# Performance work log

Measured on AMD Instinct MI355X. Metric: run time of the kernel, lower is better.

Reference implementation:

```python
import jax, jax.numpy as jnp
import numpy as np

N = 4096            # num nodes
D = 256             # feature dim
NUM_SUPER_NODES = 6
THRESHOLD = 0.0
EPS = 1e-10
DENSITY = 0.02      # pre-symmetrization edge density


def setup_inputs() -> dict:
    key = jax.random.key(0)
    kx, ka = jax.random.split(key)
    X = jax.random.normal(kx, (N, D), dtype=jnp.float32)
    U = jax.random.uniform(ka, (N, N), dtype=jnp.float32)
    A = (U < DENSITY).astype(jnp.float32)
    A = jnp.maximum(A, A.T)                      # symmetric 0/1 adjacency
    A = A * (1.0 - jnp.eye(N, dtype=jnp.float32))  # no self-loops
    return {"X": X, "A": A}


def _greedy_labels(sim_np, n, num_super, threshold):
    """Sequential greedy union-find merge over pairs sorted by similarity.
    Matches torch: stable descending sort on sim only; merge until
    n - merged <= num_super; relabel roots in first-occurrence order.
    Inherently sequential/data-dependent -> done in numpy on concrete values
    (the torch original also detaches via .item())."""
    iu, ju = np.triu_indices(n, k=1)
    sims = sim_np[iu, ju]
    keep = sims >= threshold
    iu, ju, sims = iu[keep], ju[keep], sims[keep]
    order = np.argsort(-sims, kind="stable")     # stable desc == list.sort(reverse=True)
    parent = np.arange(n)

    def find(i):
        while parent[i] != i:
            parent[i] = parent[parent[i]]        # path halving
            i = parent[i]
        return i

    merged = 0
    for k in order:
        pi, pj = find(int(iu[k])), find(int(ju[k]))
        if pi != pj:
            parent[pj] = pi
            merged += 1
            if n - merged <= num_super:
                break
    mapping = {}
    labels = np.empty(n, dtype=np.int64)
    nl = 0
    for i in range(n):
        r = find(i)
        if r not in mapping:
            mapping[r] = nl
            nl += 1
        labels[i] = mapping[r]
    return labels, nl


def _build_P(A):
    """Vectorized pairwise Jaccard (replaces O(n^2) python loop) + greedy merge."""
    n = A.shape[0]
    A_bin = (A > 0).astype(jnp.float32)
    deg = A_bin.sum(axis=1)                      # |N(i)|
    inter = A_bin @ A_bin.T                      # [n,n] pairwise |Ni & Nj|
    union = deg[:, None] + deg[None, :] - inter  # |Ni | Nj|
    sim = jnp.where(union > 0, inter / jnp.maximum(union, 1.0), 0.0)
    labels, m = _greedy_labels(np.asarray(sim), n, NUM_SUPER_NODES, THRESHOLD)
    P_prime = jax.nn.one_hot(jnp.asarray(labels), m, dtype=jnp.float32)  # [n, m]
    sizes = P_prime.sum(axis=0)
    return P_prime / jnp.sqrt(sizes + EPS)[None, :]   # P = P' @ diag(1/sqrt(sizes+eps))


def reference(X, A):
    P = _build_P(A)                               # [n, m], m == NUM_SUPER_NODES
    X_coarse = P.T @ X                            # [m, D]
    A_coarse = P.T @ A @ P                        # [m, m]
    return (X_coarse, A_coarse, P)
```

## Files before the change

### kernel.cpp

```cpp
#include <hip/hip_runtime.h>

typedef unsigned long long u64;
typedef unsigned short u16;
typedef unsigned char u8;

#define NN 4096
#define NCH 64
#define NSUP 6

__device__ __forceinline__ u64 gkey(int v, int u, unsigned sb) {
  int i = v < u ? v : u, j = v < u ? u : v;
  unsigned idx = (unsigned)i * (unsigned)(2 * NN - i - 1) / 2u + (unsigned)(j - i - 1);
  return ((u64)sb << 24) | (u64)(0xFFFFFFu - idx);
}

__device__ __forceinline__ void ins4(u64& a0, u64& a1, u64& a2, u64& a3, u64 kk) {
  bool g0 = kk > a0, g1 = kk > a1, g2 = kk > a2, g3 = kk > a3;
  a3 = g3 ? (g2 ? a2 : kk) : a3;
  a2 = g2 ? (g1 ? a1 : kk) : a2;
  a1 = g1 ? (g0 ? a0 : kk) : a1;
  a0 = g0 ? kk : a0;
}

__global__ __launch_bounds__(256) void k_packdeg(const float* __restrict__ A,
                                                 u64* __restrict__ bits,
                                                 u16* __restrict__ deg,
                                                 float* out, int out_n,
                                                 int* comp, int* ncomp, int* mstcnt) {
  int t = threadIdx.x;
  int w = t >> 6, lane = t & 63;
  int row = blockIdx.x * 4 + w;
  const float* rp = A + (size_t)row * NN;
  u64 my = 0;
  int dsum = 0;
#pragma unroll 8
  for (int k = 0; k < 64; ++k) {
    float v = rp[k * 64 + lane];
    u64 m = __ballot(v > 0.0f);
    dsum += __popcll(m);
    if (lane == k) my = m;
  }
  bits[(size_t)row * NCH + lane] = my;
  if (lane == 0) deg[row] = (u16)dsum;
  int g = blockIdx.x * 256 + t;
  if (g < out_n) out[g] = 0.0f;
  if (g < NN) comp[g] = g;
  if (g == 0) { *ncomp = NN; *mstcnt = 0; }
}

__global__ __launch_bounds__(256) void k_inter(const u64* __restrict__ bits,
                                               u8* __restrict__ inter) {
  __shared__ ulonglong2 L[2][64 * 16];
  int b = blockIdx.x;
  int by = (int)((129.0f - sqrtf(16641.0f - 8.0f * (float)b)) * 0.5f) - 1;
  if (by < 0) by = 0;
#define CUM(y) (64 * (y) - ((y) * ((y) - 1)) / 2)
  while (by < 63 && CUM(by + 1) <= b) ++by;
  while (CUM(by) > b) --by;
  int bx = by + (b - CUM(by));
#undef CUM
  int i0 = by * 64, j0 = bx * 64;
  int t = threadIdx.x;
  int tx = t & 15, ty = t >> 4;
  int rowA[4], swA[4], rowB[4], swB[4];
#pragma unroll
  for (int a = 0; a < 4; ++a) {
    rowA[a] = ty * 4 + a; swA[a] = (rowA[a] ^ (rowA[a] >> 2)) & 7;
    rowB[a] = tx * 4 + a; swB[a] = (rowB[a] ^ (rowB[a] >> 2)) & 7;
  }
  int cuL = t & 15, rg = t >> 4;
  int acc[4][4] = {};
  for (int st = 0; st < 2; ++st) {
    __syncthreads();
#pragma unroll
    for (int rr = 0; rr < 4; ++rr) {
      int row = rg * 4 + rr;
      int sw = (row ^ (row >> 2)) & 7;
      L[0][row * 16 + (cuL ^ sw)] =
          reinterpret_cast<const ulonglong2*>(bits + (size_t)(i0 + row) * NCH)[st * 16 + cuL];
      L[1][row * 16 + (cuL ^ sw)] =
          reinterpret_cast<const ulonglong2*>(bits + (size_t)(j0 + row) * NCH)[st * 16 + cuL];
    }
    __syncthreads();
    for (int cu = 0; cu < 16; ++cu) {
      ulonglong2 av[4], bv[4];
#pragma unroll
      for (int a = 0; a < 4; ++a) av[a] = L[0][rowA[a] * 16 + (cu ^ swA[a])];
#pragma unroll
      for (int b2 = 0; b2 < 4; ++b2) bv[b2] = L[1][rowB[b2] * 16 + (cu ^ swB[b2])];
#pragma unroll
      for (int a = 0; a < 4; ++a)
#pragma unroll
        for (int b2 = 0; b2 < 4; ++b2)
          acc[a][b2] += __popcll(av[a].x & bv[b2].x) + __popcll(av[a].y & bv[b2].y);
    }
  }
#pragma unroll
  for (int a = 0; a < 4; ++a) {
    int i = i0 + ty * 4 + a;
    uchar4 wv;
    wv.x = (u8)acc[a][0]; wv.y = (u8)acc[a][1];
    wv.z = (u8)acc[a][2]; wv.w = (u8)acc[a][3];
    *reinterpret_cast<uchar4*>(inter + (size_t)i * NN + j0 + tx * 4) = wv;
  }
  if (bx != by) {
#pragma unroll
    for (int b2 = 0; b2 < 4; ++b2) {
      int j = j0 + tx * 4 + b2;
      uchar4 wv;
      wv.x = (u8)acc[0][b2]; wv.y = (u8)acc[1][b2];
      wv.z = (u8)acc[2][b2]; wv.w = (u8)acc[3][b2];
      *reinterpret_cast<uchar4*>(inter + (size_t)j * NN + i0 + ty * 4) = wv;
    }
  }
}

__global__ __launch_bounds__(256) void k_scan0(const u8* __restrict__ inter,
                                               const u16* __restrict__ deg,
                                               u64* __restrict__ tk,
                                               u64* __restrict__ nkey,
                                               int* __restrict__ nu) {
  __shared__ u16 deg_s[NN];
  int t = threadIdx.x;
  for (int i = t; i < NN / 8; i += 256)
    reinterpret_cast<uint4*>(deg_s)[i] = reinterpret_cast<const uint4*>(deg)[i];
  __syncthreads();
  int w = t >> 6, lane = t & 63;
  int v = blockIdx.x * 4 + w;
  int dv = (int)deg_s[v];
  const u8* row = inter + (size_t)v * NN;
  u64 a0 = 0, a1 = 0, a2 = 0, a3 = 0;
  for (int it = 0; it < 4; ++it) {
    int ub = it * 1024 + lane * 16;
    uint4 pv = *reinterpret_cast<const uint4*>(row + ub);
    uint4 dg0 = reinterpret_cast<const uint4*>(deg_s)[ub >> 3];
    uint4 dg1 = reinterpret_cast<const uint4*>(deg_s)[(ub >> 3) + 1];
    unsigned pw[4] = { pv.x, pv.y, pv.z, pv.w };
    unsigned dw[8] = { dg0.x, dg0.y, dg0.z, dg0.w, dg1.x, dg1.y, dg1.z, dg1.w };
#pragma unroll
    for (int k = 0; k < 16; ++k) {
      int u = ub + k;
      int iv = (int)((pw[k >> 2] >> ((k & 3) * 8)) & 0xFF);
      int du = (int)((dw[k >> 1] >> ((k & 1) * 16)) & 0xFFFF);
      int un = dv + du - iv;
      float s = (un > 0) ? ((float)iv / (float)un) : 0.0f;
      u64 kk = (u != v)
                   ? (((u64)__float_as_uint(s) << 32) | (u64)(0xFFFFFFFFu - (unsigned)u))
                   : 0ull;
      ins4(a0, a1, a2, a3, kk);
    }
  }
#pragma unroll
  for (int off = 1; off < 64; off <<= 1) {
    u64 b0 = __shfl_xor(a0, off, 64);
    u64 b1 = __shfl_xor(a1, off, 64);
    u64 b2 = __shfl_xor(a2, off, 64);
    u64 b3 = __shfl_xor(a3, off, 64);
    ins4(a0, a1, a2, a3, b0);
    ins4(a0, a1, a2, a3, b1);
    ins4(a0, a1, a2, a3, b2);
    ins4(a0, a1, a2, a3, b3);
  }
  if (lane == 0) {
    u64* tv = tk + (size_t)v * 4;
    tv[0] = a0; tv[1] = a1; tv[2] = a2; tv[3] = a3;
    int u0 = (int)(0xFFFFFFFFu - (unsigned)(a0 & 0xFFFFFFFFull));
    nkey[v] = gkey(v, u0, (unsigned)(a0 >> 32));
    nu[v] = u0;
  }
}

__global__ __launch_bounds__(256) void k_scan(const u8* __restrict__ inter,
                                              const u16* __restrict__ deg,
                                              const u64* __restrict__ tk,
                                              const int* __restrict__ comp,
                                              const int* __restrict__ ncomp,
                                              u64* __restrict__ nkey,
                                              int* __restrict__ nu) {
  if (*ncomp <= 1) return;
  __shared__ u16 comp_s[NN];
  __shared__ u16 deg_s[NN];
  __shared__ int anyneed;
  int t = threadIdx.x;
  if (t == 0) anyneed = 0;
  for (int i = t; i < NN / 8; i += 256) {
    int4 ca = reinterpret_cast<const int4*>(comp)[i * 2];
    int4 cb = reinterpret_cast<const int4*>(comp)[i * 2 + 1];
    uint4 pk;
    pk.x = (unsigned)ca.x | ((unsigned)ca.y << 16);
    pk.y = (unsigned)ca.z | ((unsigned)ca.w << 16);
    pk.z = (unsigned)cb.x | ((unsigned)cb.y << 16);
    pk.w = (unsigned)cb.z | ((unsigned)cb.w << 16);
    reinterpret_cast<uint4*>(comp_s)[i] = pk;
  }
  __syncthreads();
  int w = t >> 6, lane = t & 63;
  int v = blockIdx.x * 4 + w;
  int cv = (int)comp_s[v];
  u64 gk = 0; int bu = -1; bool need = true;
  const u64* tv = tk + (size_t)v * 4;
#pragma unroll
  for (int e = 0; e < 4; ++e) {
    u64 cand = tv[e];
    unsigned uu = 0xFFFFFFFFu - (unsigned)(cand & 0xFFFFFFFFull);
    if (need && (int)comp_s[uu] != cv) {
      need = false;
      gk = gkey(v, (int)uu, (unsigned)(cand >> 32));
      bu = (int)uu;
    }
  }
  if (!need) {
    if (lane == 0) { nkey[v] = gk; nu[v] = bu; }
  } else if (lane == 0) {
    atomicOr(&anyneed, 1 << w);
  }
  __syncthreads();
  int needmask = anyneed;
  if (!needmask) return;
  for (int i = t; i < NN / 8; i += 256)
    reinterpret_cast<uint4*>(deg_s)[i] = reinterpret_cast<const uint4*>(deg)[i];
  __syncthreads();
  if (!(needmask >> w & 1)) return;
  int dv = (int)deg_s[v];
  const u8* row = inter + (size_t)v * NN;
  u64 key = 0;
  for (int it = 0; it < 4; ++it) {
    int ub = it * 1024 + lane * 16;
    uint4 pv = *reinterpret_cast<const uint4*>(row + ub);
    uint4 dg0 = reinterpret_cast<const uint4*>(deg_s)[ub >> 3];
    uint4 dg1 = reinterpret_cast<const uint4*>(deg_s)[(ub >> 3) + 1];
    uint4 cs0 = reinterpret_cast<const uint4*>(comp_s)[ub >> 3];
    uint4 cs1 = reinterpret_cast<const uint4*>(comp_s)[(ub >> 3) + 1];
    unsigned pw[4] = { pv.x, pv.y, pv.z, pv.w };
    unsigned dw[8] = { dg0.x, dg0.y, dg0.z, dg0.w, dg1.x, dg1.y, dg1.z, dg1.w };
    unsigned cw[8] = { cs0.x, cs0.y, cs0.z, cs0.w, cs1.x, cs1.y, cs1.z, cs1.w };
#pragma unroll
    for (int k = 0; k < 16; ++k) {
      int iv = (int)((pw[k >> 2] >> ((k & 3) * 8)) & 0xFF);
      int du = (int)((dw[k >> 1] >> ((k & 1) * 16)) & 0xFFFF);
      int cu = (int)((cw[k >> 1] >> ((k & 1) * 16)) & 0xFFFF);
      int un = dv + du - iv;
      float s = (un > 0) ? ((float)iv / (float)un) : 0.0f;
      u64 kk = (cu != cv)
                   ? (((u64)__float_as_uint(s) << 32) | (u64)(0xFFFFFFFFu - (unsigned)(ub + k)))
                   : 0ull;
      if (kk > key) key = kk;
    }
  }
#pragma unroll
  for (int off = 32; off > 0; off >>= 1) {
    unsigned lo = (unsigned)key, hi = (unsigned)(key >> 32);
    unsigned olo = __shfl_xor(lo, off, 64), ohi = __shfl_xor(hi, off, 64);
    u64 o = ((u64)ohi << 32) | (u64)olo;
    if (o > key) key = o;
  }
  if (lane == 0) {
    u64 pk = 0; int u = -1;
    if (key != 0ull) {
      unsigned simb = (unsigned)(key >> 32);
      u = (int)(0xFFFFFFFFu - (unsigned)(key & 0xFFFFFFFFull));
      pk = gkey(v, u, simb);
    }
    nkey[v] = pk; nu[v] = u;
  }
}

__global__ __launch_bounds__(1024) void k_merge(const u64* __restrict__ nkey,
                                                const int* __restrict__ nu,
                                                int* comp, int* ncomp, int* mstcnt,
                                                u64* mkey, int* mi, int* mj,
                                                int* labels_g, float* invs_g, float* out) {
  if (*ncomp <= 1) return;
  __shared__ int parent_s[NN];
  __shared__ u64 cbest_s[NN];
  __shared__ unsigned char mk_s[NN];
  __shared__ int roots[16];
  __shared__ int rcnt, cnt_s, chg_s, changed;
  __shared__ int szs[8];
  __shared__ float ivs[8];
  int t = threadIdx.x;
  for (int c = t; c < NN; c += 1024) { parent_s[c] = c; cbest_s[c] = 0ull; }
  __syncthreads();
  for (int v = t; v < NN; v += 1024) {
    u64 k = nkey[v];
    if (k) atomicMax(&cbest_s[comp[v]], k);
  }
  __syncthreads();
  for (int v = t; v < NN; v += 1024) {
    u64 k = nkey[v];
    if (!k) continue;
    int c = comp[v];
    if (k == cbest_s[c]) {
      int u = nu[v];
      int cu = comp[u];
      bool mutual = (cbest_s[cu] == k);
      if (!mutual || v < u) {
        int slot = atomicAdd(mstcnt, 1);
        if (slot < 4352) { mkey[slot] = k; mi[slot] = v; mj[slot] = u; }
      }
      parent_s[c] = cu;
    }
  }
  __syncthreads();
  for (int c = t; c < NN; c += 1024) {
    int pc = parent_s[c];
    if (parent_s[pc] == c && c < pc) parent_s[c] = c;
  }
  __syncthreads();
  for (int it = 0; it < 13; ++it) {
    if (t == 0) chg_s = 0;
    __syncthreads();
    for (int c = t; c < NN; c += 1024) {
      int p1 = parent_s[c], p2 = parent_s[p1];
      if (p1 != p2) { parent_s[c] = p2; chg_s = 1; }
    }
    __syncthreads();
    if (!chg_s) break;
  }
  for (int c = t; c < NN; c += 1024) mk_s[c] = 0;
  if (t == 0) cnt_s = 0;
  __syncthreads();
  for (int v = t; v < NN; v += 1024) {
    int nc = parent_s[comp[v]];
    comp[v] = nc;
    mk_s[nc] = 1;
  }
  __syncthreads();
  int lc = 0;
  for (int c = t; c < NN; c += 1024) lc += mk_s[c];
  atomicAdd(&cnt_s, lc);
  __syncthreads();
  if (t == 0) *ncomp = cnt_s;
  __syncthreads();
  if (cnt_s != 1) return;
  int* rr = reinterpret_cast<int*>(cbest_s);
  u64* rk = cbest_s + 2048;
  int* rs = reinterpret_cast<int*>(cbest_s + 3072);
  int nm = *mstcnt;
  if (nm < 0) nm = 0;
  if (nm > 4352) nm = 4352;
  for (int v = t; v < NN; v += 1024) parent_s[v] = v;
  for (int pass = 0; pass < NSUP - 1; ++pass) {
    u64 bk = ~0ull; int bsel = -1;
    for (int e = t; e < nm; e += 1024) { u64 k = mkey[e]; if (k < bk) { bk = k; bsel = e; } }
    rk[t] = bk; rs[t] = bsel;
    __syncthreads();
    for (int s = 512; s > 0; s >>= 1) {
      if (t < s && rk[t + s] < rk[t]) { rk[t] = rk[t + s]; rs[t] = rs[t + s]; }
      __syncthreads();
    }
    if (t == 0 && rs[0] >= 0) mkey[rs[0]] = ~0ull;
    __syncthreads();
  }
  for (int round = 0; round < 64; ++round) {
    if (t == 0) changed = 0;
    __syncthreads();
    for (int e = t; e < nm; e += 1024) {
      if (mkey[e] == ~0ull) continue;
      int a = parent_s[mi[e]], b = parent_s[mj[e]];
      if (a == b) continue;
      int m = a < b ? a : b, M = a < b ? b : a;
      int old = atomicMin(&parent_s[M], m);
      if (old > m) changed = 1;
    }
    __syncthreads();
    for (int rep = 0; rep < 3; ++rep) {
      for (int v = t; v < NN; v += 1024) parent_s[v] = parent_s[parent_s[v]];
      __syncthreads();
    }
    int ch = changed;
    __syncthreads();
    if (!ch) break;
  }
  for (int rep = 0; rep < 13; ++rep) {
    for (int v = t; v < NN; v += 1024) parent_s[v] = parent_s[parent_s[v]];
    __syncthreads();
  }
  if (t == 0) rcnt = 0;
  __syncthreads();
  for (int v = t; v < NN; v += 1024)
    if (parent_s[v] == v) { int s = atomicAdd(&rcnt, 1); if (s < 16) roots[s] = v; }
  __syncthreads();
  if (t == 0) {
    int c = rcnt > 16 ? 16 : rcnt;
    for (int a = 1; a < c; ++a) {
      int x = roots[a]; int b2 = a - 1;
      while (b2 >= 0 && roots[b2] > x) { roots[b2 + 1] = roots[b2]; --b2; }
      roots[b2 + 1] = x;
    }
  }
  if (t < 8) szs[t] = 0;
  __syncthreads();
  if (t < rcnt && t < 16) rr[roots[t]] = t;
  __syncthreads();
  for (int v = t; v < NN; v += 1024) {
    int lab = rr[parent_s[v]];
    labels_g[v] = lab;
    atomicAdd(&szs[lab], 1);
  }
  __syncthreads();
  if (t < rcnt && t < 8) {
    float iv = 1.0f / sqrtf((float)szs[t] + 1e-10f);
    ivs[t] = iv; invs_g[t] = iv;
  }
  __syncthreads();
  for (int v = t; v < NN; v += 1024) {
    int lab = rr[parent_s[v]];
    float* base = out + 1572 + v * 6;
#pragma unroll
    for (int b2 = 0; b2 < 6; ++b2) base[b2] = (b2 == lab) ? ivs[lab] : 0.0f;
  }
}

__global__ __launch_bounds__(256) void k_coarse(const float* __restrict__ X,
                                                const u64* __restrict__ bits,
                                                const int* __restrict__ labels,
                                                const float* __restrict__ invs,
                                                float* out) {
  int t = threadIdx.x;
  if (blockIdx.x < 64) {
    __shared__ float acc[6][256];
    __shared__ int labs[64];
    __shared__ float ivl[64];
#pragma unroll
    for (int m = 0; m < 6; ++m) acc[m][t] = 0.0f;
    if (t < 64) { int v = blockIdx.x * 64 + t; int l = labels[v]; labs[t] = l; ivl[t] = invs[l]; }
    __syncthreads();
    int v0 = blockIdx.x * 64;
    for (int r = 0; r < 64; ++r) {
      float x = X[(size_t)(v0 + r) * 256 + t];
      acc[labs[r]][t] += ivl[r] * x;
    }
    __syncthreads();
#pragma unroll
    for (int m = 0; m < 6; ++m) atomicAdd(&out[m * 256 + t], acc[m][t]);
  } else {
    __shared__ unsigned char labs8[NN];
    __shared__ float accA[36];
    __shared__ float ivsl[8];
    for (int v = t; v < NN; v += 256) labs8[v] = (unsigned char)labels[v];
    if (t < 36) accA[t] = 0.0f;
    if (t < 6) ivsl[t] = invs[t];
    __syncthreads();
    int i = (blockIdx.x - 64) * 256 + t;
    u64 cnt = 0;
    const u64* row = bits + (size_t)i * NCH;
    for (int c = 0; c < NCH; ++c) {
      u64 wm = row[c];
      while (wm) {
        int j = (c << 6) + __builtin_ctzll(wm);
        wm &= wm - 1;
        cnt += 1ull << (labs8[j] * 10);
      }
    }
    int li = labs8[i];
    float fi = ivsl[li];
#pragma unroll
    for (int b = 0; b < 6; ++b) {
      float cb = (float)((cnt >> (b * 10)) & 1023ull);
      if (cb != 0.0f) atomicAdd(&accA[li * 6 + b], fi * ivsl[b] * cb);
    }
    __syncthreads();
    if (t < 36) atomicAdd(&out[1536 + t], accA[t]);
  }
}

extern "C" void kernel_launch(void* const* d_in, const int* in_sizes, int n_in,
                              void* d_out, int out_size, void* d_ws, size_t ws_size,
                              hipStream_t stream) {
  const float* X = (const float*)d_in[0];
  const float* A = (const float*)d_in[1];
  float* out = (float*)d_out;

  char* wp = (char*)d_ws;
  size_t off = 0;
#define WALLOC(ty, name, count) \
  ty* name = (ty*)(wp + off);   \
  off += (((size_t)(count) * sizeof(ty)) + 255) & ~(size_t)255;
  WALLOC(u64, bits, (size_t)NN * NCH)
  WALLOC(u8, inter, (size_t)NN * NN)
  WALLOC(u16, deg, NN)
  WALLOC(u64, tk, (size_t)NN * 4)
  WALLOC(int, comp, NN)
  WALLOC(u64, nkey, NN)
  WALLOC(int, nu, NN)
  WALLOC(u64, mkey, 4352)
  WALLOC(int, mi, 4352)
  WALLOC(int, mj, 4352)
  WALLOC(int, labels, NN)
  WALLOC(float, invs, 8)
  WALLOC(int, ncomp, 1)
  WALLOC(int, mstcnt, 1)
#undef WALLOC
  if (off > ws_size) return;

  k_packdeg<<<NN / 4, 256, 0, stream>>>(A, bits, deg, out, out_size, comp, ncomp, mstcnt);
  k_inter<<<2080, 256, 0, stream>>>(bits, inter);
  k_scan0<<<NN / 4, 256, 0, stream>>>(inter, deg, tk, nkey, nu);
  for (int ph = 0; ph < 12; ++ph) {
    k_merge<<<1, 1024, 0, stream>>>(nkey, nu, comp, ncomp, mstcnt, mkey, mi, mj,
                                    labels, invs, out);
    if (ph < 11)
      k_scan<<<NN / 4, 256, 0, stream>>>(inter, deg, tk, comp, ncomp, nkey, nu);
  }
  k_coarse<<<80, 256, 0, stream>>>(X, bits, labels, invs, out);
}
```

Measured before the change: 364.1 us.

## Slim Boruvka merge kernel and skip shared-memory staging in scan fast path

k_scan now checks each node's cached top-4 candidates straight from global memory using lane 0, and loads the comp/deg arrays into shared memory only when some node in the block needs a full row rescan. k_merge drops from 1024 to 256 threads and packs component and parent arrays into 16-bit shared storage. It also replaces the byte mark array with a 64-word bitmask counted by popcount. The intent is to cut per-phase fixed costs such as shared-memory fills and block startup. The trade-off is fewer threads per loop in the merge kernel and scattered global reads in the scan fast path.

```diff
diff --git a/kernel.cpp b/kernel.cpp
--- a/kernel.cpp
+++ b/kernel.cpp
@@ -180,9 +180,31 @@
   if (*ncomp <= 1) return;
   __shared__ u16 comp_s[NN];
   __shared__ u16 deg_s[NN];
-  __shared__ int anyneed;
+  __shared__ int needflag;
   int t = threadIdx.x;
-  if (t == 0) anyneed = 0;
+  int w = t >> 6, lane = t & 63;
+  int v = blockIdx.x * 4 + w;
+  if (t == 0) needflag = 0;
+  __syncthreads();
+  if (lane == 0) {
+    int cv = comp[v];
+    const u64* tv = tk + (size_t)v * 4;
+    u64 gk = 0; int bu = -1;
+#pragma unroll
+    for (int e = 0; e < 4; ++e) {
+      u64 cand = tv[e];
+      unsigned uu = 0xFFFFFFFFu - (unsigned)(cand & 0xFFFFFFFFull);
+      if (bu < 0 && comp[uu] != cv) {
+        bu = (int)uu;
+        gk = gkey(v, (int)uu, (unsigned)(cand >> 32));
+      }
+    }
+    if (bu >= 0) { nkey[v] = gk; nu[v] = bu; }
+    else atomicOr(&needflag, 1 << w);
+  }
+  __syncthreads();
+  int needmask = needflag;
+  if (!needmask) return;
   for (int i = t; i < NN / 8; i += 256) {
     int4 ca = reinterpret_cast<const int4*>(comp)[i * 2];
     int4 cb = reinterpret_cast<const int4*>(comp)[i * 2 + 1];
@@ -192,35 +214,11 @@
     pk.z = (unsigned)cb.x | ((unsigned)cb.y << 16);
     pk.w = (unsigned)cb.z | ((unsigned)cb.w << 16);
     reinterpret_cast<uint4*>(comp_s)[i] = pk;
-  }
-  __syncthreads();
-  int w = t >> 6, lane = t & 63;
-  int v = blockIdx.x * 4 + w;
+    reinterpret_cast<uint4*>(deg_s)[i] = reinterpret_cast<const uint4*>(deg)[i];
+  }
+  __syncthreads();
+  if (!(needmask >> w & 1)) return;
   int cv = (int)comp_s[v];
-  u64 gk = 0; int bu = -1; bool need = true;
-  const u64* tv = tk + (size_t)v * 4;
-#pragma unroll
-  for (int e = 0; e < 4; ++e) {
-    u64 cand = tv[e];
-    unsigned uu = 0xFFFFFFFFu - (unsigned)(cand & 0xFFFFFFFFull);
-    if (need && (int)comp_s[uu] != cv) {
-      need = false;
-      gk = gkey(v, (int)uu, (unsigned)(cand >> 32));
-      bu = (int)uu;
-    }
-  }
-  if (!need) {
-    if (lane == 0) { nkey[v] = gk; nu[v] = bu; }
-  } else if (lane == 0) {
-    atomicOr(&anyneed, 1 << w);
-  }
-  __syncthreads();
-  int needmask = anyneed;
-  if (!needmask) return;
-  for (int i = t; i < NN / 8; i += 256)
-    reinterpret_cast<uint4*>(deg_s)[i] = reinterpret_cast<const uint4*>(deg)[i];
-  __syncthreads();
-  if (!(needmask >> w & 1)) return;
   int dv = (int)deg_s[v];
   const u8* row = inter + (size_t)v * NN;
   u64 key = 0;
@@ -265,87 +263,98 @@
   }
 }
 
-__global__ __launch_bounds__(1024) void k_merge(const u64* __restrict__ nkey,
-                                                const int* __restrict__ nu,
-                                                int* comp, int* ncomp, int* mstcnt,
-                                                u64* mkey, int* mi, int* mj,
-                                                int* labels_g, float* invs_g, float* out) {
+__global__ __launch_bounds__(256) void k_merge(const u64* __restrict__ nkey,
+                                               const int* __restrict__ nu,
+                                               int* comp, int* ncomp, int* mstcnt,
+                                               u64* mkey, int* mi, int* mj,
+                                               int* labels_g, float* invs_g, float* out) {
   if (*ncomp <= 1) return;
-  __shared__ int parent_s[NN];
-  __shared__ u64 cbest_s[NN];
-  __shared__ unsigned char mk_s[NN];
+  __shared__ u16 comp16[NN];
+  __shared__ u16 parent16[NN];
+  __shared__ u64 cbest[NN];
+  __shared__ u64 mark64[64];
   __shared__ int roots[16];
   __shared__ int rcnt, cnt_s, chg_s, changed;
   __shared__ int szs[8];
   __shared__ float ivs[8];
   int t = threadIdx.x;
-  for (int c = t; c < NN; c += 1024) { parent_s[c] = c; cbest_s[c] = 0ull; }
-  __syncthreads();
-  for (int v = t; v < NN; v += 1024) {
+  for (int i = t; i < NN / 8; i += 256) {
+    int4 ca = reinterpret_cast<const int4*>(comp)[i * 2];
+    int4 cb = reinterpret_cast<const int4*>(comp)[i * 2 + 1];
+    uint4 pk;
+    pk.x = (unsigned)ca.x | ((unsigned)ca.y << 16);
+    pk.y = (unsigned)ca.z | ((unsigned)ca.w << 16);
+    pk.z = (unsigned)cb.x | ((unsigned)cb.y << 16);
+    pk.w = (unsigned)cb.z | ((unsigned)cb.w << 16);
+    reinterpret_cast<uint4*>(comp16)[i] = pk;
+  }
+  for (int c = t; c < NN; c += 256) { cbest[c] = 0ull; parent16[c] = (u16)c; }
+  __syncthreads();
+  for (int v = t; v < NN; v += 256) {
     u64 k = nkey[v];
-    if (k) atomicMax(&cbest_s[comp[v]], k);
-  }
-  __syncthreads();
-  for (int v = t; v < NN; v += 1024) {
+    if (k) atomicMax(&cbest[(int)comp16[v]], k);
+  }
+  __syncthreads();
+  for (int v = t; v < NN; v += 256) {
     u64 k = nkey[v];
     if (!k) continue;
-    int c = comp[v];
-    if (k == cbest_s[c]) {
+    int c = (int)comp16[v];
+    if (k == cbest[c]) {
       int u = nu[v];
-      int cu = comp[u];
-      bool mutual = (cbest_s[cu] == k);
+      int cu = (int)comp16[u];
+      bool mutual = (cbest[cu] == k);
       if (!mutual || v < u) {
         int slot = atomicAdd(mstcnt, 1);
         if (slot < 4352) { mkey[slot] = k; mi[slot] = v; mj[slot] = u; }
       }
-      parent_s[c] = cu;
-    }
-  }
-  __syncthreads();
-  for (int c = t; c < NN; c += 1024) {
-    int pc = parent_s[c];
-    if (parent_s[pc] == c && c < pc) parent_s[c] = c;
+      parent16[c] = (u16)cu;
+    }
+  }
+  __syncthreads();
+  for (int c = t; c < NN; c += 256) {
+    int pc = (int)parent16[c];
+    if ((int)parent16[pc] == c && c < pc) parent16[c] = (u16)c;
   }
   __syncthreads();
   for (int it = 0; it < 13; ++it) {
     if (t == 0) chg_s = 0;
     __syncthreads();
-    for (int c = t; c < NN; c += 1024) {
-      int p1 = parent_s[c], p2 = parent_s[p1];
-      if (p1 != p2) { parent_s[c] = p2; chg_s = 1; }
+    for (int c = t; c < NN; c += 256) {
+      int p1 = (int)parent16[c], p2 = (int)parent16[p1];
+      if (p1 != p2) { parent16[c] = (u16)p2; chg_s = 1; }
     }
     __syncthreads();
     if (!chg_s) break;
   }
-  for (int c = t; c < NN; c += 1024) mk_s[c] = 0;
+  if (t < 64) mark64[t] = 0ull;
   if (t == 0) cnt_s = 0;
   __syncthreads();
-  for (int v = t; v < NN; v += 1024) {
-    int nc = parent_s[comp[v]];
+  for (int v = t; v < NN; v += 256) {
+    int nc = (int)parent16[(int)comp16[v]];
     comp[v] = nc;
-    mk_s[nc] = 1;
-  }
-  __syncthreads();
-  int lc = 0;
-  for (int c = t; c < NN; c += 1024) lc += mk_s[c];
-  atomicAdd(&cnt_s, lc);
+    atomicOr(&mark64[nc >> 6], 1ull << (nc & 63));
+  }
+  __syncthreads();
+  if (t < 64) atomicAdd(&cnt_s, __popcll(mark64[t]));
   __syncthreads();
   if (t == 0) *ncomp = cnt_s;
   __syncthreads();
   if (cnt_s != 1) return;
-  int* rr = reinterpret_cast<int*>(cbest_s);
-  u64* rk = cbest_s + 2048;
-  int* rs = reinterpret_cast<int*>(cbest_s + 3072);
+  int* p32 = reinterpret_cast<int*>(cbest);
+  u64* rk = cbest + 2048;
+  int* rs = reinterpret_cast<int*>(cbest + 2560);
+  u16* rr16 = parent16;
   int nm = *mstcnt;
   if (nm < 0) nm = 0;
   if (nm > 4352) nm = 4352;
-  for (int v = t; v < NN; v += 1024) parent_s[v] = v;
+  for (int v = t; v < NN; v += 256) p32[v] = v;
+  __syncthreads();
   for (int pass = 0; pass < NSUP - 1; ++pass) {
     u64 bk = ~0ull; int bsel = -1;
-    for (int e = t; e < nm; e += 1024) { u64 k = mkey[e]; if (k < bk) { bk = k; bsel = e; } }
+    for (int e = t; e < nm; e += 256) { u64 k = mkey[e]; if (k < bk) { bk = k; bsel = e; } }
     rk[t] = bk; rs[t] = bsel;
     __syncthreads();
-    for (int s = 512; s > 0; s >>= 1) {
+    for (int s = 128; s > 0; s >>= 1) {
       if (t < s && rk[t + s] < rk[t]) { rk[t] = rk[t + s]; rs[t] = rs[t + s]; }
       __syncthreads();
     }
@@ -355,17 +364,17 @@
   for (int round = 0; round < 64; ++round) {
     if (t == 0) changed = 0;
     __syncthreads();
-    for (int e = t; e < nm; e += 1024) {
+    for (int e = t; e < nm; e += 256) {
       if (mkey[e] == ~0ull) continue;
-      int a = parent_s[mi[e]], b = parent_s[mj[e]];
+      int a = p32[mi[e]], b = p32[mj[e]];
       if (a == b) continue;
       int m = a < b ? a : b, M = a < b ? b : a;
-      int old = atomicMin(&parent_s[M], m);
+      int old = atomicMin(&p32[M], m);
       if (old > m) changed = 1;
     }
     __syncthreads();
     for (int rep = 0; rep < 3; ++rep) {
-      for (int v = t; v < NN; v += 1024) parent_s[v] = parent_s[parent_s[v]];
+      for (int v = t; v < NN; v += 256) p32[v] = p32[p32[v]];
       __syncthreads();
     }
     int ch = changed;
@@ -373,13 +382,13 @@
     if (!ch) break;
   }
   for (int rep = 0; rep < 13; ++rep) {
-    for (int v = t; v < NN; v += 1024) parent_s[v] = parent_s[parent_s[v]];
+    for (int v = t; v < NN; v += 256) p32[v] = p32[p32[v]];
     __syncthreads();
   }
   if (t == 0) rcnt = 0;
   __syncthreads();
-  for (int v = t; v < NN; v += 1024)
-    if (parent_s[v] == v) { int s = atomicAdd(&rcnt, 1); if (s < 16) roots[s] = v; }
+  for (int v = t; v < NN; v += 256)
+    if (p32[v] == v) { int s = atomicAdd(&rcnt, 1); if (s < 16) roots[s] = v; }
   __syncthreads();
   if (t == 0) {
     int c = rcnt > 16 ? 16 : rcnt;
@@ -391,10 +400,10 @@
   }
   if (t < 8) szs[t] = 0;
   __syncthreads();
-  if (t < rcnt && t < 16) rr[roots[t]] = t;
-  __syncthreads();
-  for (int v = t; v < NN; v += 1024) {
-    int lab = rr[parent_s[v]];
+  if (t < rcnt && t < 16) rr16[roots[t]] = (u16)t;
+  __syncthreads();
+  for (int v = t; v < NN; v += 256) {
+    int lab = (int)rr16[p32[v]];
     labels_g[v] = lab;
     atomicAdd(&szs[lab], 1);
   }
@@ -404,8 +413,8 @@
     ivs[t] = iv; invs_g[t] = iv;
   }
   __syncthreads();
-  for (int v = t; v < NN; v += 1024) {
-    int lab = rr[parent_s[v]];
+  for (int v = t; v < NN; v += 256) {
+    int lab = (int)rr16[p32[v]];
     float* base = out + 1572 + v * 6;
 #pragma unroll
     for (int b2 = 0; b2 < 6; ++b2) base[b2] = (b2 == lab) ? ivs[lab] : 0.0f;
@@ -498,8 +507,8 @@
   k_inter<<<2080, 256, 0, stream>>>(bits, inter);
   k_scan0<<<NN / 4, 256, 0, stream>>>(inter, deg, tk, nkey, nu);
   for (int ph = 0; ph < 12; ++ph) {
-    k_merge<<<1, 1024, 0, stream>>>(nkey, nu, comp, ncomp, mstcnt, mkey, mi, mj,
-                                    labels, invs, out);
+    k_merge<<<1, 256, 0, stream>>>(nkey, nu, comp, ncomp, mstcnt, mkey, mi, mj,
+                                   labels, invs, out);
     if (ph < 11)
       k_scan<<<NN / 4, 256, 0, stream>>>(inter, deg, tk, comp, ncomp, nkey, nu);
   }
```

After: 485.1 us. 33.2% more time.
